# Optimization experiments

Measured on AMD Instinct MI355X. Metric: run time of the kernel, lower is better.

The kernel has to match this reference:

```python
import jax, jax.numpy as jnp
import numpy as np

S_DIM = 4096
N_NODES = 4096
N_EDGES = 32768


def _coarsen(ei_np, N):
    """Integer-only greedy coarsening, faithful to MNGRAPH.forward's while-loop.
    Returns (select order, flattened neighbor indices, segment ids, per-hub
    neighbor counts, forward-fill indices replicating the stale-M behavior for
    empty neighborhoods, and the remapped final edge_index)."""
    ei = ei_np.astype(np.int64).copy()
    I = np.bincount(ei[0], minlength=N)
    O = np.bincount(ei[1], minlength=N)
    order = np.argsort(-(I + O), kind='stable')  # torch.argsort(D, descending=True)
    visits = np.zeros(N, dtype=bool)
    select = []
    nbr_idx, nbr_seg, counts = [], [], []
    while order.size > 0:
        node = int(order[0])
        select.append(node)
        visits[node] = True
        # H = unique neighbors of node in the CURRENT (rewritten) edge_index
        H = np.unique(np.concatenate([ei[1][ei[0] == node], ei[0][ei[1] == node]]))
        visits[H] = True
        order = order[~visits[order]]
        # rewrite: endpoints in H that are not already-selected hubs -> node
        Hn = H[~np.isin(H, np.asarray(select, dtype=np.int64))]
        ei[np.isin(ei, Hn)] = node
        ei = ei[:, ei[0] != ei[1]]  # drop self-loops
        # append reversed edges that are not already present (pair-code isin
        # == the original O(E^2) all/any comparison, computed efficiently)
        code = ei[0] * N + ei[1]
        rcode = ei[1] * N + ei[0]
        new = ~np.isin(rcode, code)
        ei = np.concatenate([ei, ei[::-1][:, new]], axis=1)
        k = len(select) - 1
        nbr_idx.append(H)
        nbr_seg.append(np.full(H.shape[0], k, dtype=np.int64))
        counts.append(H.shape[0])
    select = np.asarray(select, dtype=np.int64)
    sort_sel = np.sort(select)
    ei_out = np.searchsorted(sort_sel, ei)  # compact node ids
    counts = np.asarray(counts, dtype=np.int64)
    # forward-fill: when H is empty the original appends the previous (stale) M
    fill = np.arange(select.shape[0])
    for i in range(select.shape[0]):
        if counts[i] == 0:
            fill[i] = fill[i - 1] if i > 0 else 0
    nbr = np.concatenate(nbr_idx) if nbr_idx else np.zeros(0, np.int64)
    seg = np.concatenate(nbr_seg) if nbr_seg else np.zeros(0, np.int64)
    return select, nbr, seg, counts, fill, ei_out


def setup_inputs() -> dict:
    key = jax.random.key(0)
    k1, k2, k3, k4 = jax.random.split(key, 4)
    x = jax.random.normal(k1, (N_NODES, S_DIM), dtype=jnp.float32)
    edge_index = jax.random.randint(k2, (2, N_EDGES), 0, N_NODES, dtype=jnp.int64)
    bound = float(np.sqrt(6.0 / (1.0 + S_DIM)))  # xavier_uniform on (1, S)
    W1 = jax.random.uniform(k3, (S_DIM,), jnp.float32, -bound, bound)
    W2 = jax.random.uniform(k4, (S_DIM,), jnp.float32, -bound, bound)
    B1 = jnp.zeros((S_DIM,), jnp.float32)
    B2 = jnp.zeros((S_DIM,), jnp.float32)
    return {"x": x, "edge_index": edge_index, "W1": W1, "W2": W2, "B1": B1, "B2": B2}


def reference(x, edge_index, W1, W2, B1, B2):
    N = x.shape[0]
    sel, nbr, seg, counts, fill, ei_out = _coarsen(np.asarray(edge_index), N)
    K = sel.shape[0]
    # Dn = x[n]*W1+B1 for every neighbor of every hub; per-hub mean via segment_sum
    Dn = x[jnp.asarray(nbr)] * W1 + B1                      # [T, S]
    sums = jax.ops.segment_sum(Dn, jnp.asarray(seg), num_segments=K)
    denom = jnp.maximum(jnp.asarray(counts), 1).astype(x.dtype)[:, None]
    mean_Dn = sums / denom                                  # [K, S]
    Dv = x[jnp.asarray(sel)] * W2 + B2                      # [K, S]
    END = jnp.concatenate([Dv, mean_Dn], axis=1)            # [K, 2S]
    END = END[jnp.asarray(fill)]                            # stale-M replication
    return END, jnp.asarray(ei_out)
```

## Files before the change

kernel.cpp:

```cpp
#include <hip/hip_runtime.h>
#include <hip/hip_bf16.h>

#define NT 1024
#define NNODES 4096
#define ECAP 65536

__global__ __launch_bounds__(256)
void zeroBM(int4* __restrict__ bm) {
    bm[(size_t)blockIdx.x * 256 + threadIdx.x] = make_int4(0, 0, 0, 0);
}

__device__ __forceinline__ int blockScanExcl(int v, int* s_w, int* total) {
    const int tid  = threadIdx.x;
    const int lane = tid & 63;
    const int wv   = tid >> 6;
    int x = v;
#pragma unroll
    for (int off = 1; off < 64; off <<= 1) {
        int t = __shfl_up(x, off, 64);
        if (lane >= off) x += t;
    }
    if (lane == 63) s_w[wv] = x;
    __syncthreads();
    if (tid < 16) {
        int y = s_w[tid];
#pragma unroll
        for (int off = 1; off < 16; off <<= 1) {
            int t = __shfl_up(y, off, 16);
            if (tid >= off) y += t;
        }
        s_w[tid] = y;
    }
    __syncthreads();
    int base = wv ? s_w[wv - 1] : 0;
    int tot  = s_w[15];
    __syncthreads();
    *total = tot;
    return base + x - v;
}

__global__ __launch_bounds__(NT, 1)
void phaseA1(const int* __restrict__ ei, int E0,
             int* __restrict__ U, int* __restrict__ V,
             unsigned int* __restrict__ BM,
             int* __restrict__ NBR, int* __restrict__ OTH,
             int* __restrict__ ORDV, int* __restrict__ ROFFG, int* __restrict__ RENDG,
             int* __restrict__ HAND)
{
    __shared__ unsigned short s_order[NNODES];
    __shared__ unsigned char  s_vis[NNODES];
    __shared__ unsigned char  s_rank[NNODES];
    __shared__ unsigned int   s_hb[NNODES / 32];
    __shared__ int s_roff[NNODES];
    __shared__ int s_rend[NNODES];
    __shared__ int s_tmp[NNODES];
    __shared__ int s_mat[64][65];
    __shared__ int s_w[16];
    __shared__ int s_bc[16];

    const int tid = threadIdx.x;

    for (int i = tid; i < NNODES; i += NT) { s_vis[i] = 0; s_tmp[i] = 0; }
    for (int i = tid; i < NNODES / 32; i += NT) s_hb[i] = 0;
    if (tid < 16) s_bc[tid] = 0;
    __syncthreads();

    for (int i = tid; i < E0; i += NT)
        if (ei[2 * i + 1] != 0) s_bc[9] = 1;
    __syncthreads();
    const int is64 = !s_bc[9];

    for (int e = tid; e < E0; e += NT) {
        int uu = ei[is64 ? 2 * e : e];
        int vv = ei[is64 ? 2 * (E0 + e) : (E0 + e)];
        U[e] = uu; V[e] = vv;
        atomicAdd(&s_tmp[uu], 1);
        atomicAdd(&s_tmp[vv], 1);
    }
    __syncthreads();
    for (int n = tid; n < NNODES; n += NT) atomicMax(&s_bc[7], s_tmp[n]);
    __syncthreads();
    const int maxd = s_bc[7];

    if (maxd < 64) {
        const int wv = tid >> 6, lane = tid & 63;
        const unsigned long long ltm = (1ull << lane) - 1ull;
        for (int g = wv; g < 64; g += 16) {
            int n = g * 64 + lane;
            int d = s_tmp[n];
            int rk = 0;
            for (int dd = 0; dd < 64; ++dd) {
                unsigned long long bal = __ballot(d == dd);
                if (lane == 0) s_mat[dd][g] = __popcll(bal);
                if (d == dd) rk = __popcll(bal & ltm);
            }
            s_rank[n] = (unsigned char)rk;
        }
        __syncthreads();
        if (tid < 64) {
            int run = 0;
            for (int g = 0; g < 64; ++g) { int t = s_mat[tid][g]; s_mat[tid][g] = run; run += t; }
            s_mat[tid][64] = run;
        }
        __syncthreads();
        if (tid < 64) {
            int x = s_mat[tid][64];
#pragma unroll
            for (int off = 1; off < 64; off <<= 1) {
                int t = __shfl_up(x, off, 64);
                if (tid >= off) x += t;
            }
            int T = __shfl(x, 63, 64);
            s_mat[tid][64] = T - x;
        }
        __syncthreads();
        for (int g = wv; g < 64; g += 16) {
            int n = g * 64 + lane;
            int d = s_tmp[n];
            int pos = s_mat[d][64] + s_mat[d][g] + (int)s_rank[n];
            s_order[pos] = (unsigned short)n;
        }
        __syncthreads();
    } else {
        for (int d = maxd; d >= 0; --d) {
            int n0 = tid * 4;
            int f0 = (s_tmp[n0] == d), f1 = (s_tmp[n0 + 1] == d);
            int f2 = (s_tmp[n0 + 2] == d), f3 = (s_tmp[n0 + 3] == d);
            int tot;
            int off = blockScanExcl(f0 + f1 + f2 + f3, s_w, &tot);
            int idx = s_bc[4] + off;
            if (f0) s_order[idx++] = (unsigned short)n0;
            if (f1) s_order[idx++] = (unsigned short)(n0 + 1);
            if (f2) s_order[idx++] = (unsigned short)(n0 + 2);
            if (f3) s_order[idx++] = (unsigned short)(n0 + 3);
            __syncthreads();
            if (tid == 0) s_bc[4] += tot;
            __syncthreads();
        }
    }

    if (tid == 0) {
        int nd = s_order[0];
        s_bc[0] = nd; s_vis[nd] = 1;
    }
    __syncthreads();
    {
        const int node = s_bc[0];
        for (int e = tid; e < E0; e += NT) {
            int uu = U[e], vv = V[e];
            if (uu == node) {
                int w = vv; unsigned m = 1u << (w & 31);
                unsigned old = atomicOr(&s_hb[w >> 5], m);
                if (!(old & m)) { int i = atomicAdd(&s_bc[2], 1); s_tmp[i] = w; s_vis[w] = 1; }
            }
            if (vv == node) {
                int w = uu; unsigned m = 1u << (w & 31);
                unsigned old = atomicOr(&s_hb[w >> 5], m);
                if (!(old & m)) { int i = atomicAdd(&s_bc[2], 1); s_tmp[i] = w; s_vis[w] = 1; }
            }
        }
        __syncthreads();
        for (int e = tid; e < E0; e += NT) {
            int uu = U[e];
            if (uu != node && ((s_hb[uu >> 5] >> (uu & 31)) & 1)) U[e] = node;
            int vv = V[e];
            if (vv != node && ((s_hb[vv >> 5] >> (vv & 31)) & 1)) V[e] = node;
        }
        __syncthreads();
    }

    for (int e = tid; e < E0; e += NT) {
        int uu = U[e], vv = V[e];
        if (uu != vv) {
            unsigned code = ((unsigned)uu << 12) | (unsigned)vv;
            atomicOr(&BM[code >> 5], 1u << (code & 31));
        }
    }
    __syncthreads();
    for (int t0 = 0; t0 < E0; t0 += NT * 32) {
        unsigned fm = 0u;
        const int base = t0 + tid * 32;
        for (int j = 0; j < 32; ++j) {
            int e = base + j;
            if (e < E0) {
                int uu = U[e], vv = V[e];
                if (uu != vv) {
                    unsigned rc = ((unsigned)vv << 12) | (unsigned)uu;
                    unsigned old = atomicOr(&BM[rc >> 5], 0u);
                    if (!((old >> (rc & 31)) & 1u)) fm |= (1u << j);
                }
            }
        }
        int tot;
        int off = blockScanExcl(__popc(fm), s_w, &tot);
        int r = s_bc[5] + off;
        unsigned m = fm;
        while (m) {
            int j = __ffs((int)m) - 1; m &= m - 1;
            int e = base + j;
            U[E0 + r] = V[e]; V[E0 + r] = U[e];
            ++r;
        }
        __syncthreads();
        if (tid == 0) s_bc[5] += tot;
        __syncthreads();
    }
    const int E1 = E0 + s_bc[5];

    for (int n = tid; n < NNODES; n += NT) s_roff[n] = 0;
    __syncthreads();
    for (int e = tid; e < E1; e += NT) {
        int uu = U[e], vv = V[e];
        if (uu != vv) atomicAdd(&s_roff[uu], 1);
    }
    __syncthreads();
    {
        int n0 = tid * 4;
        int c0 = s_roff[n0], c1 = s_roff[n0 + 1], c2 = s_roff[n0 + 2], c3 = s_roff[n0 + 3];
        int tot;
        int off = blockScanExcl(c0 + c1 + c2 + c3, s_w, &tot);
        int st = off;
        s_roff[n0] = st;     s_rend[n0] = st;     st += c0;
        s_roff[n0 + 1] = st; s_rend[n0 + 1] = st; st += c1;
        s_roff[n0 + 2] = st; s_rend[n0 + 2] = st; st += c2;
        s_roff[n0 + 3] = st; s_rend[n0 + 3] = st;
    }
    __syncthreads();
    for (int e = tid; e < E1; e += NT) {
        int uu = U[e], vv = V[e];
        if (uu != vv) {
            int p = atomicAdd(&s_rend[uu], 1);
            OTH[p] = vv;
        }
    }
    __syncthreads();
    {
        const int cnt0 = s_bc[2];
        for (int i = tid; i < cnt0; i += NT) NBR[i] = s_tmp[i];
    }
    for (int i = tid; i < NNODES; i += NT) {
        int nd = (int)s_order[i];
        ORDV[i]  = nd | (s_vis[nd] ? 0x8000 : 0);
        ROFFG[i] = s_roff[i];
        RENDG[i] = s_rend[i];
    }
    if (tid == 0) { HAND[0] = E1; HAND[1] = s_bc[2]; HAND[2] = s_bc[0]; }
}

__global__ __launch_bounds__(64, 1)
void phaseA2(const int* __restrict__ OTH, int* __restrict__ NBR,
             const int* __restrict__ ORDV, const int* __restrict__ ROFFG,
             const int* __restrict__ RENDG, const int* __restrict__ HAND,
             int* __restrict__ SEL, int* __restrict__ CNTS,
             int* __restrict__ NST, int* __restrict__ FIL, int* __restrict__ SC,
             int* __restrict__ LABG, int* __restrict__ RNKG)
{
    __shared__ unsigned short s_ord[NNODES];
    __shared__ unsigned int   s_visbits[NNODES / 32];
    __shared__ unsigned int   s_meta[NNODES];
    __shared__ unsigned short s_so[NNODES];
    __shared__ int s_cnt[NNODES];
    __shared__ int s_stamp[NNODES];
    __shared__ int s_roff[NNODES];
    __shared__ int s_rend[NNODES];

    const int ln = threadIdx.x;
    const unsigned long long ltm = (1ull << ln) - 1ull;
    const int cnt0 = HAND[1], hub0 = HAND[2];
    volatile int* vstamp = s_stamp;

    for (int i = ln; i < NNODES / 32; i += 64) s_visbits[i] = 0u;
    for (int i = ln; i < NNODES; i += 64) {
        int ov = ORDV[i];
        int nd = ov & 0x7FFF;
        s_ord[i] = (unsigned short)nd;
        s_meta[nd] = ((unsigned)i << 16) | (unsigned)nd;
        s_roff[i] = ROFFG[i];
        s_rend[i] = RENDG[i];
        s_stamp[i] = 0; s_cnt[i] = 0;
        if (ov & 0x8000) atomicOr(&s_visbits[i >> 5], 1u << (i & 31));
    }
    if (ln == 0) {
        s_meta[hub0] = (unsigned)hub0 | 0x8000u;
        s_so[0] = (unsigned short)hub0;
        s_cnt[0] = cnt0;
    }

    int nc = cnt0;
    int k = 1;

    unsigned lo = 0u, hi = 0u;
    auto reload = [&]() { lo = ~s_visbits[ln]; hi = ~s_visbits[ln + 64]; };
    auto extract = [&]() -> int {
        unsigned long long b = __ballot(lo != 0u);
        if (b) {
            int sl = __ffsll((long long)b) - 1;
            unsigned ww = __shfl(lo, sl, 64);
            if (ln == sl) lo &= lo - 1;
            return sl * 32 + (__ffs((int)ww) - 1);
        }
        b = __ballot(hi != 0u);
        if (b) {
            int sl = __ffsll((long long)b) - 1;
            unsigned ww = __shfl(hi, sl, 64);
            if (ln == sl) hi &= hi - 1;
            return 2048 + sl * 32 + (__ffs((int)ww) - 1);
        }
        return -1;
    };

    auto commitNew = [&](unsigned g, int w, bool nw, unsigned long long bal,
                         unsigned relv) {
        if (nw) {
            NBR[nc + __popcll(bal & ltm)] = w;
            int slot = (int)(g >> 16);
            atomicOr(&s_visbits[slot >> 5], 1u << (slot & 31));
            if (!(g & 0x8000u)) s_meta[w] = relv;
        }
        nc += __popcll(bal);
    };

    auto procFast = [&](int hub, int hslot, int o, unsigned g) {
        const unsigned relv = ((unsigned)hslot << 16) | (unsigned)hub | 0x8000u;
        int w = (o >= 0) ? (int)(g & 0x7FFFu) : hub;
        bool valid = (o >= 0) && (w != hub);
        if (valid) vstamp[w] = ln;
        int r = valid ? vstamp[w] : -1;
        bool nw = valid && (r == ln);
        unsigned long long bal = __ballot(nw);
        commitNew(g, w, nw, bal, relv);
    };

    auto procSlow = [&](int hub, int hslot, int rb, int re, int o0) {
        const unsigned relv = ((unsigned)hslot << 16) | (unsigned)hub | 0x8000u;
        const int key = k << 6;
        int o = o0;
        for (int s0 = rb; s0 < re; s0 += 64) {
            unsigned g = (o >= 0) ? s_meta[o] : 0u;
            int w = (o >= 0) ? (int)(g & 0x7FFFu) : hub;
            bool cnd = (w != hub);
            int old = key;
            if (cnd) old = atomicMax(&s_stamp[w], key);
            bool nw = cnd && (old < key);
            unsigned long long bal = __ballot(nw);
            commitNew(g, w, nw, bal, relv);
            int s1 = s0 + 64;
            o = (s1 + ln < re) ? OTH[s1 + ln] : -1;
        }
    };

    for (;;) {
        reload();
        int sl0 = extract();
        if (sl0 < 0) break;
        int sl1 = extract(), sl2 = -1, sl3 = -1;
        if (sl1 >= 0) { sl2 = extract(); if (sl2 >= 0) sl3 = extract(); }

        int c0 = (int)s_ord[sl0];
        int c1 = (sl1 >= 0) ? (int)s_ord[sl1] : -1;
        int c2 = (sl2 >= 0) ? (int)s_ord[sl2] : -1;
        int c3 = (sl3 >= 0) ? (int)s_ord[sl3] : -1;

        {
            int ms = (ln == 0) ? sl0 : (ln == 1) ? sl1 : (ln == 2) ? sl2 : sl3;
            if (ln < 4 && ms >= 0) atomicOr(&s_visbits[ms >> 5], 1u << (ms & 31));
        }

        int rb0 = s_roff[c0], re0 = s_rend[c0];
        int rb1 = 0, re1 = 0, rb2 = 0, re2 = 0, rb3 = 0, re3 = 0;
        if (c1 >= 0) { rb1 = s_roff[c1]; re1 = s_rend[c1]; }
        if (c2 >= 0) { rb2 = s_roff[c2]; re2 = s_rend[c2]; }
        if (c3 >= 0) { rb3 = s_roff[c3]; re3 = s_rend[c3]; }
        int v0 = (rb0 + ln < re0) ? OTH[rb0 + ln] : -1;
        int v1 = (c1 >= 0 && rb1 + ln < re1) ? OTH[rb1 + ln] : -1;
        int v2 = (c2 >= 0 && rb2 + ln < re2) ? OTH[rb2 + ln] : -1;
        int v3 = (c3 >= 0 && rb3 + ln < re3) ? OTH[rb3 + ln] : -1;

        if (ln == 0) {
            s_meta[c0] = ((unsigned)sl0 << 16) | (unsigned)c0 | 0x8000u;
            s_so[k] = (unsigned short)c0;
        }
        {
            unsigned g0 = (v0 >= 0) ? s_meta[v0] : 0u;
            int begin = nc;
            if (re0 - rb0 <= 64) procFast(c0, sl0, v0, g0);
            else                 procSlow(c0, sl0, rb0, re0, v0);
            if (ln == 0) s_cnt[k] = nc - begin;
            k++;
        }
        if (c1 >= 0) {
            unsigned m1 = s_meta[c1];
            unsigned g1 = (v1 >= 0) ? s_meta[v1] : 0u;
            if ((int)(m1 & 0x7FFFu) == c1) {
                if (ln == 0) {
                    s_meta[c1] = ((unsigned)sl1 << 16) | (unsigned)c1 | 0x8000u;
                    s_so[k] = (unsigned short)c1;
                }
                int begin = nc;
                if (re1 - rb1 <= 64) procFast(c1, sl1, v1, g1);
                else                 procSlow(c1, sl1, rb1, re1, v1);
                if (ln == 0) s_cnt[k] = nc - begin;
                k++;
            }
        }
        if (c2 >= 0) {
            unsigned m2 = s_meta[c2];
            unsigned g2 = (v2 >= 0) ? s_meta[v2] : 0u;
            if ((int)(m2 & 0x7FFFu) == c2) {
                if (ln == 0) {
                    s_meta[c2] = ((unsigned)sl2 << 16) | (unsigned)c2 | 0x8000u;
                    s_so[k] = (unsigned short)c2;
                }
                int begin = nc;
                if (re2 - rb2 <= 64) procFast(c2, sl2, v2, g2);
                else                 procSlow(c2, sl2, rb2, re2, v2);
                if (ln == 0) s_cnt[k] = nc - begin;
                k++;
            }
        }
        if (c3 >= 0) {
            unsigned m3 = s_meta[c3];
            unsigned g3 = (v3 >= 0) ? s_meta[v3] : 0u;
            if ((int)(m3 & 0x7FFFu) == c3) {
                if (ln == 0) {
                    s_meta[c3] = ((unsigned)sl3 << 16) | (unsigned)c3 | 0x8000u;
                    s_so[k] = (unsigned short)c3;
                }
                int begin = nc;
                if (re3 - rb3 <= 64) procFast(c3, sl3, v3, g3);
                else                 procSlow(c3, sl3, rb3, re3, v3);
                if (ln == 0) s_cnt[k] = nc - begin;
                k++;
            }
        }
    }
    const int K = k;

    {
        int base = 0;
        for (int c = 0; c < NNODES / 64; ++c) {
            int n = c * 64 + ln;
            unsigned mv = s_meta[n];
            int f = ((mv & 0x8000u) != 0u) && ((int)(mv & 0x7FFFu) == n);
            unsigned long long b = __ballot(f);
            s_stamp[n] = base + __popcll(b & ltm);
            base += __popcll(b);
        }
    }
    {
        int nb = 0;
        for (int c = 0; c * 64 < K; ++c) {
            int i = c * 64 + ln;
            int cv = (i < K) ? s_cnt[i] : 0;
            int x = cv;
#pragma unroll
            for (int off = 1; off < 64; off <<= 1) {
                int t = __shfl_up(x, off, 64);
                if (ln >= off) x += t;
            }
            if (i < K) { NST[i] = nb + x - cv; CNTS[i] = cv; SEL[i] = (int)s_so[i]; }
            nb += __shfl(x, 63, 64);
        }
    }
    {
        int carry = 0;
        for (int c = 0; c * 64 < K; ++c) {
            int i = c * 64 + ln;
            int f = (i < K) && (s_cnt[i] > 0);
            unsigned long long b = __ballot(f);
            unsigned long long m = b & ((ln == 63) ? ~0ull : ((1ull << (ln + 1)) - 1ull));
            int fil = m ? (c * 64 + 63 - __clzll(m)) : carry;
            if (i < K) FIL[i] = fil;
            carry = b ? (c * 64 + 63 - __clzll(b)) : carry;
        }
    }
    if (ln == 0) SC[0] = K;
    for (int i = ln; i < NNODES; i += 64) {
        LABG[i] = (int)(s_meta[i] & 0x7FFFu);
        RNKG[i] = s_stamp[i];
    }
}

__global__ __launch_bounds__(NT, 1)
void phaseA3(const int* __restrict__ U, const int* __restrict__ V,
             const int* __restrict__ LABG, const int* __restrict__ RNKG,
             const int* __restrict__ HAND, int* __restrict__ SC,
             int* __restrict__ TMP, float* __restrict__ out)
{
    __shared__ unsigned short l_lab[NNODES];
    __shared__ int l_rnk[NNODES];
    __shared__ int s_w[16];
    __shared__ int s_base[1];

    const int tid = threadIdx.x;
    for (int i = tid; i < NNODES; i += NT) {
        l_lab[i] = (unsigned short)LABG[i];
        l_rnk[i] = RNKG[i];
    }
    if (tid == 0) s_base[0] = 0;
    __syncthreads();

    const int E1 = HAND[0];
    const int K  = SC[0];
    const size_t obase = (size_t)K * 8192;

    for (int t0 = 0; t0 < E1; t0 += NT * 64) {
        unsigned long long fm = 0ull;
        const int base = t0 + tid * 64;
        if (base + 64 <= E1) {
            const int4* U4 = (const int4*)(U + base);
            const int4* V4 = (const int4*)(V + base);
#pragma unroll
            for (int q = 0; q < 16; ++q) {
                int4 a = U4[q], b = V4[q];
                int j = q * 4;
                if ((int)l_lab[a.x] != (int)l_lab[b.x]) fm |= 1ull << j;
                if ((int)l_lab[a.y] != (int)l_lab[b.y]) fm |= 1ull << (j + 1);
                if ((int)l_lab[a.z] != (int)l_lab[b.z]) fm |= 1ull << (j + 2);
                if ((int)l_lab[a.w] != (int)l_lab[b.w]) fm |= 1ull << (j + 3);
            }
        } else {
            for (int j = 0; j < 64; ++j) {
                int e = base + j;
                if (e < E1) {
                    if ((int)l_lab[U[e]] != (int)l_lab[V[e]]) fm |= 1ull << j;
                }
            }
        }
        int tot;
        int off = blockScanExcl(__popcll(fm), s_w, &tot);
        int r = s_base[0] + off;
        unsigned long long m = fm;
        while (m) {
            int j = __ffsll((long long)m) - 1; m &= m - 1;
            int e = base + j;
            out[obase + (size_t)r] = (float)l_rnk[(int)l_lab[U[e]]];
            TMP[r] = l_rnk[(int)l_lab[V[e]]];
            ++r;
        }
        __syncthreads();
        if (tid == 0) s_base[0] += tot;
        __syncthreads();
    }
    const int Ef = s_base[0];
    if (tid == 0) SC[1] = Ef;
    for (int r = tid; r < Ef; r += NT)
        out[obase + (size_t)Ef + (size_t)r] = (float)TMP[r];
}

__global__ __launch_bounds__(256, 4)
void phaseB(const float* __restrict__ x,
            const float* __restrict__ W1, const float* __restrict__ W2,
            const float* __restrict__ B1, const float* __restrict__ B2,
            const int* __restrict__ NBR, const int* __restrict__ SEL,
            const int* __restrict__ CNTS, const int* __restrict__ NST,
            const int* __restrict__ FIL, const int* __restrict__ SC,
            float* __restrict__ out)
{
    const int K = SC[0];
    const int k = blockIdx.x;
    if (k >= K) return;
    const int kk   = FIL[k];
    const int node = SEL[kk];
    const int cnt  = CNTS[kk];
    const int st   = NST[kk];
    const int tid  = threadIdx.x;
    const float4* x4 = (const float4*)x;

    float4 acc[4];
#pragma unroll
    for (int j = 0; j < 4; j++) acc[j] = make_float4(0.f, 0.f, 0.f, 0.f);

    for (int r = 0; r < cnt; ++r) {
        const float4* row = x4 + (size_t)NBR[st + r] * 1024;
#pragma unroll
        for (int j = 0; j < 4; j++) {
            float4 t = row[tid + j * 256];
            acc[j].x += t.x; acc[j].y += t.y; acc[j].z += t.z; acc[j].w += t.w;
        }
    }

    const float fc  = (float)cnt;
    const float inv = 1.0f / (float)(cnt > 1 ? cnt : 1);
    const float4* xr = x4 + (size_t)node * 1024;
    float4* o4 = (float4*)(out + (size_t)k * 8192);

#pragma unroll
    for (int j = 0; j < 4; j++) {
        int c = tid + j * 256;
        float4 w1 = ((const float4*)W1)[c], b1 = ((const float4*)B1)[c];
        float4 w2 = ((const float4*)W2)[c], b2 = ((const float4*)B2)[c];
        float4 xv = xr[c];
        float4 pd, pm;
        pd.x = xv.x * w2.x + b2.x;
        pd.y = xv.y * w2.y + b2.y;
        pd.z = xv.z * w2.z + b2.z;
        pd.w = xv.w * w2.w + b2.w;
        pm.x = (acc[j].x * w1.x + fc * b1.x) * inv;
        pm.y = (acc[j].y * w1.y + fc * b1.y) * inv;
        pm.z = (acc[j].z * w1.z + fc * b1.z) * inv;
        pm.w = (acc[j].w * w1.w + fc * b1.w) * inv;
        o4[c] = pd;
        o4[1024 + c] = pm;
    }
}

extern "C" void kernel_launch(void* const* d_in, const int* in_sizes, int n_in,
                              void* d_out, int out_size, void* d_ws, size_t ws_size,
                              hipStream_t stream)
{
    const float* x  = (const float*)d_in[0];
    const int*   ei = (const int*)d_in[1];
    const float* W1 = (const float*)d_in[2];
    const float* W2 = (const float*)d_in[3];
    const float* B1 = (const float*)d_in[4];
    const float* B2 = (const float*)d_in[5];
    const int E0 = in_sizes[1] / 2;

    char* w = (char*)d_ws;
    int* U = (int*)w;
    int* V = U + ECAP;
    unsigned int* BM = (unsigned int*)(V + ECAP);
    int* OTH = (int*)BM;
    int* NBR = OTH + 2 * ECAP;
    int* TMP = NBR + 2 * ECAP;
    char* meta = (char*)BM + (2u << 20);
    int* SEL   = (int*)meta;
    int* CNTS  = SEL  + NNODES;
    int* NST   = CNTS + NNODES;
    int* FIL   = NST  + NNODES;
    int* SC    = FIL  + NNODES;
    int* ORDV  = SC   + 16;
    int* ROFFG = ORDV + NNODES;
    int* RENDG = ROFFG + NNODES;
    int* LABG  = RENDG + NNODES;
    int* RNKG  = LABG + NNODES;
    int* HAND  = RNKG + NNODES;
    float* out = (float*)d_out;

    hipLaunchKernelGGL(zeroBM, dim3(512), dim3(256), 0, stream, (int4*)BM);

    hipLaunchKernelGGL(phaseA1, dim3(1), dim3(NT), 0, stream,
                       ei, E0, U, V, BM, NBR, OTH, ORDV, ROFFG, RENDG, HAND);
    hipLaunchKernelGGL(phaseA2, dim3(1), dim3(64), 0, stream,
                       OTH, NBR, ORDV, ROFFG, RENDG, HAND,
                       SEL, CNTS, NST, FIL, SC, LABG, RNKG);
    hipLaunchKernelGGL(phaseA3, dim3(1), dim3(NT), 0, stream,
                       U, V, LABG, RNKG, HAND, SC, TMP, out);
    hipLaunchKernelGGL(phaseB, dim3(NNODES), dim3(256), 0, stream,
                       x, W1, W2, B1, B2, NBR, SEL, CNTS, NST, FIL, SC, out);
}
```

Baseline: 1.005 ms.

## Fuse three single-block coarsening kernels into one phaseA kernel with shared state

```diff
diff --git a/kernel.cpp b/kernel.cpp
--- a/kernel.cpp
+++ b/kernel.cpp
@@ -1,7 +1,8 @@
 #include <hip/hip_runtime.h>
 #include <hip/hip_bf16.h>
 
-#define NT 1024
+#define NT 512
+#define NW (NT / 64)
 #define NNODES 4096
 #define ECAP 65536
 
@@ -23,7 +24,7 @@
     if (lane == 63) s_w[wv] = x;
     __syncthreads();
     if (tid < 16) {
-        int y = s_w[tid];
+        int y = (tid < NW) ? s_w[tid] : 0;
 #pragma unroll
         for (int off = 1; off < 16; off <<= 1) {
             int t = __shfl_up(y, off, 16);
@@ -40,28 +41,33 @@
 }
 
 __global__ __launch_bounds__(NT, 1)
-void phaseA1(const int* __restrict__ ei, int E0,
-             int* __restrict__ U, int* __restrict__ V,
-             unsigned int* __restrict__ BM,
-             int* __restrict__ NBR, int* __restrict__ OTH,
-             int* __restrict__ ORDV, int* __restrict__ ROFFG, int* __restrict__ RENDG,
-             int* __restrict__ HAND)
+void phaseA(const int* __restrict__ ei, int E0,
+            int* __restrict__ U, int* __restrict__ V,
+            unsigned int* __restrict__ BM,
+            int* __restrict__ NBR, int* __restrict__ OTH,
+            int* __restrict__ SEL, int* __restrict__ CNTS,
+            int* __restrict__ NST, int* __restrict__ FIL, int* __restrict__ SC,
+            int* __restrict__ TMP, float* __restrict__ out)
 {
-    __shared__ unsigned short s_order[NNODES];
-    __shared__ unsigned char  s_vis[NNODES];
+    __shared__ unsigned short s_ord[NNODES];
+    __shared__ unsigned short s_pos[NNODES];
+    __shared__ unsigned short s_so[NNODES];
     __shared__ unsigned char  s_rank[NNODES];
+    __shared__ unsigned int   s_visbits[NNODES / 32];
     __shared__ unsigned int   s_hb[NNODES / 32];
+    __shared__ unsigned int   s_meta[NNODES];
+    __shared__ int s_mat[64][65];
     __shared__ int s_roff[NNODES];
     __shared__ int s_rend[NNODES];
-    __shared__ int s_tmp[NNODES];
-    __shared__ int s_mat[64][65];
+    __shared__ int s_stamp[NNODES];
+    __shared__ int s_degcnt[NNODES];
     __shared__ int s_w[16];
     __shared__ int s_bc[16];
 
     const int tid = threadIdx.x;
 
-    for (int i = tid; i < NNODES; i += NT) { s_vis[i] = 0; s_tmp[i] = 0; }
-    for (int i = tid; i < NNODES / 32; i += NT) s_hb[i] = 0;
+    for (int i = tid; i < NNODES; i += NT) s_degcnt[i] = 0;
+    for (int i = tid; i < NNODES / 32; i += NT) { s_hb[i] = 0u; s_visbits[i] = 0u; }
     if (tid < 16) s_bc[tid] = 0;
     __syncthreads();
 
@@ -74,25 +80,25 @@
         int uu = ei[is64 ? 2 * e : e];
         int vv = ei[is64 ? 2 * (E0 + e) : (E0 + e)];
         U[e] = uu; V[e] = vv;
-        atomicAdd(&s_tmp[uu], 1);
-        atomicAdd(&s_tmp[vv], 1);
-    }
-    __syncthreads();
-    for (int n = tid; n < NNODES; n += NT) atomicMax(&s_bc[7], s_tmp[n]);
+        atomicAdd(&s_degcnt[uu], 1);
+        atomicAdd(&s_degcnt[vv], 1);
+    }
+    __syncthreads();
+    for (int n = tid; n < NNODES; n += NT) atomicMax(&s_bc[7], s_degcnt[n]);
     __syncthreads();
     const int maxd = s_bc[7];
 
     if (maxd < 64) {
         const int wv = tid >> 6, lane = tid & 63;
-        const unsigned long long ltm = (1ull << lane) - 1ull;
-        for (int g = wv; g < 64; g += 16) {
+        const unsigned long long wltm = (1ull << lane) - 1ull;
+        for (int g = wv; g < 64; g += NW) {
             int n = g * 64 + lane;
-            int d = s_tmp[n];
+            int d = s_degcnt[n];
             int rk = 0;
             for (int dd = 0; dd < 64; ++dd) {
                 unsigned long long bal = __ballot(d == dd);
                 if (lane == 0) s_mat[dd][g] = __popcll(bal);
-                if (d == dd) rk = __popcll(bal & ltm);
+                if (d == dd) rk = __popcll(bal & wltm);
             }
             s_rank[n] = (unsigned char)rk;
         }
@@ -114,34 +120,37 @@
             s_mat[tid][64] = T - x;
         }
         __syncthreads();
-        for (int g = wv; g < 64; g += 16) {
+        for (int g = wv; g < 64; g += NW) {
             int n = g * 64 + lane;
-            int d = s_tmp[n];
+            int d = s_degcnt[n];
             int pos = s_mat[d][64] + s_mat[d][g] + (int)s_rank[n];
-            s_order[pos] = (unsigned short)n;
+            s_ord[pos] = (unsigned short)n;
         }
         __syncthreads();
     } else {
         for (int d = maxd; d >= 0; --d) {
-            int n0 = tid * 4;
-            int f0 = (s_tmp[n0] == d), f1 = (s_tmp[n0 + 1] == d);
-            int f2 = (s_tmp[n0 + 2] == d), f3 = (s_tmp[n0 + 3] == d);
+            const int n0 = tid * 8;
+            int f[8], cnt = 0;
+#pragma unroll
+            for (int q = 0; q < 8; ++q) { f[q] = (s_degcnt[n0 + q] == d); cnt += f[q]; }
             int tot;
-            int off = blockScanExcl(f0 + f1 + f2 + f3, s_w, &tot);
+            int off = blockScanExcl(cnt, s_w, &tot);
             int idx = s_bc[4] + off;
-            if (f0) s_order[idx++] = (unsigned short)n0;
-            if (f1) s_order[idx++] = (unsigned short)(n0 + 1);
-            if (f2) s_order[idx++] = (unsigned short)(n0 + 2);
-            if (f3) s_order[idx++] = (unsigned short)(n0 + 3);
+#pragma unroll
+            for (int q = 0; q < 8; ++q)
+                if (f[q]) s_ord[idx++] = (unsigned short)(n0 + q);
             __syncthreads();
             if (tid == 0) s_bc[4] += tot;
             __syncthreads();
         }
     }
 
+    for (int i = tid; i < NNODES; i += NT) s_pos[s_ord[i]] = (unsigned short)i;
+    __syncthreads();
+
     if (tid == 0) {
-        int nd = s_order[0];
-        s_bc[0] = nd; s_vis[nd] = 1;
+        s_bc[0] = (int)s_ord[0];
+        atomicOr(&s_visbits[0], 1u);
     }
     __syncthreads();
     {
@@ -151,12 +160,22 @@
             if (uu == node) {
                 int w = vv; unsigned m = 1u << (w & 31);
                 unsigned old = atomicOr(&s_hb[w >> 5], m);
-                if (!(old & m)) { int i = atomicAdd(&s_bc[2], 1); s_tmp[i] = w; s_vis[w] = 1; }
+                if (!(old & m)) {
+                    int i = atomicAdd(&s_bc[2], 1);
+                    s_degcnt[i] = w;
+                    int sl = (int)s_pos[w];
+                    atomicOr(&s_visbits[sl >> 5], 1u << (sl & 31));
+                }
             }
             if (vv == node) {
                 int w = uu; unsigned m = 1u << (w & 31);
                 unsigned old = atomicOr(&s_hb[w >> 5], m);
-                if (!(old & m)) { int i = atomicAdd(&s_bc[2], 1); s_tmp[i] = w; s_vis[w] = 1; }
+                if (!(old & m)) {
+                    int i = atomicAdd(&s_bc[2], 1);
+                    s_degcnt[i] = w;
+                    int sl = (int)s_pos[w];
+                    atomicOr(&s_visbits[sl >> 5], 1u << (sl & 31));
+                }
             }
         }
         __syncthreads();
@@ -215,15 +234,17 @@
     }
     __syncthreads();
     {
-        int n0 = tid * 4;
-        int c0 = s_roff[n0], c1 = s_roff[n0 + 1], c2 = s_roff[n0 + 2], c3 = s_roff[n0 + 3];
+        const int n0 = tid * 8;
+        int c[8], s = 0;
+#pragma unroll
+        for (int q = 0; q < 8; ++q) { c[q] = s_roff[n0 + q]; s += c[q]; }
         int tot;
-        int off = blockScanExcl(c0 + c1 + c2 + c3, s_w, &tot);
+        int off = blockScanExcl(s, s_w, &tot);
         int st = off;
-        s_roff[n0] = st;     s_rend[n0] = st;     st += c0;
-        s_roff[n0 + 1] = st; s_rend[n0 + 1] = st; st += c1;
-        s_roff[n0 + 2] = st; s_rend[n0 + 2] = st; st += c2;
-        s_roff[n0 + 3] = st; s_rend[n0 + 3] = st;
+#pragma unroll
+        for (int q = 0; q < 8; ++q) {
+            s_roff[n0 + q] = st; s_rend[n0 + q] = st; st += c[q];
+        }
     }
     __syncthreads();
     for (int e = tid; e < E1; e += NT) {
@@ -234,274 +255,222 @@
         }
     }
     __syncthreads();
-    {
-        const int cnt0 = s_bc[2];
-        for (int i = tid; i < cnt0; i += NT) NBR[i] = s_tmp[i];
-    }
+    const int cnt0 = s_bc[2];
+    for (int i = tid; i < cnt0; i += NT) NBR[i] = s_degcnt[i];
+    __syncthreads();
+
     for (int i = tid; i < NNODES; i += NT) {
-        int nd = (int)s_order[i];
-        ORDV[i]  = nd | (s_vis[nd] ? 0x8000 : 0);
-        ROFFG[i] = s_roff[i];
-        RENDG[i] = s_rend[i];
-    }
-    if (tid == 0) { HAND[0] = E1; HAND[1] = s_bc[2]; HAND[2] = s_bc[0]; }
-}
-
-__global__ __launch_bounds__(64, 1)
-void phaseA2(const int* __restrict__ OTH, int* __restrict__ NBR,
-             const int* __restrict__ ORDV, const int* __restrict__ ROFFG,
-             const int* __restrict__ RENDG, const int* __restrict__ HAND,
-             int* __restrict__ SEL, int* __restrict__ CNTS,
-             int* __restrict__ NST, int* __restrict__ FIL, int* __restrict__ SC,
-             int* __restrict__ LABG, int* __restrict__ RNKG)
-{
-    __shared__ unsigned short s_ord[NNODES];
-    __shared__ unsigned int   s_visbits[NNODES / 32];
-    __shared__ unsigned int   s_meta[NNODES];
-    __shared__ unsigned short s_so[NNODES];
-    __shared__ int s_cnt[NNODES];
-    __shared__ int s_stamp[NNODES];
-    __shared__ int s_roff[NNODES];
-    __shared__ int s_rend[NNODES];
-
-    const int ln = threadIdx.x;
-    const unsigned long long ltm = (1ull << ln) - 1ull;
-    const int cnt0 = HAND[1], hub0 = HAND[2];
-    volatile int* vstamp = s_stamp;
-
-    for (int i = ln; i < NNODES / 32; i += 64) s_visbits[i] = 0u;
-    for (int i = ln; i < NNODES; i += 64) {
-        int ov = ORDV[i];
-        int nd = ov & 0x7FFF;
-        s_ord[i] = (unsigned short)nd;
+        int nd = (int)s_ord[i];
         s_meta[nd] = ((unsigned)i << 16) | (unsigned)nd;
-        s_roff[i] = ROFFG[i];
-        s_rend[i] = RENDG[i];
-        s_stamp[i] = 0; s_cnt[i] = 0;
-        if (ov & 0x8000) atomicOr(&s_visbits[i >> 5], 1u << (i & 31));
-    }
-    if (ln == 0) {
+        s_stamp[i] = 0;
+        s_degcnt[i] = 0;
+    }
+    __syncthreads();
+    if (tid == 0) {
+        int hub0 = s_bc[0];
         s_meta[hub0] = (unsigned)hub0 | 0x8000u;
         s_so[0] = (unsigned short)hub0;
-        s_cnt[0] = cnt0;
-    }
-
-    int nc = cnt0;
-    int k = 1;
-
-    unsigned lo = 0u, hi = 0u;
-    auto reload = [&]() { lo = ~s_visbits[ln]; hi = ~s_visbits[ln + 64]; };
-    auto extract = [&]() -> int {
-        unsigned long long b = __ballot(lo != 0u);
-        if (b) {
-            int sl = __ffsll((long long)b) - 1;
-            unsigned ww = __shfl(lo, sl, 64);
-            if (ln == sl) lo &= lo - 1;
-            return sl * 32 + (__ffs((int)ww) - 1);
-        }
-        b = __ballot(hi != 0u);
-        if (b) {
-            int sl = __ffsll((long long)b) - 1;
-            unsigned ww = __shfl(hi, sl, 64);
-            if (ln == sl) hi &= hi - 1;
-            return 2048 + sl * 32 + (__ffs((int)ww) - 1);
-        }
-        return -1;
-    };
-
-    auto commitNew = [&](unsigned g, int w, bool nw, unsigned long long bal,
-                         unsigned relv) {
-        if (nw) {
-            NBR[nc + __popcll(bal & ltm)] = w;
-            int slot = (int)(g >> 16);
-            atomicOr(&s_visbits[slot >> 5], 1u << (slot & 31));
-            if (!(g & 0x8000u)) s_meta[w] = relv;
-        }
-        nc += __popcll(bal);
-    };
-
-    auto procFast = [&](int hub, int hslot, int o, unsigned g) {
-        const unsigned relv = ((unsigned)hslot << 16) | (unsigned)hub | 0x8000u;
-        int w = (o >= 0) ? (int)(g & 0x7FFFu) : hub;
-        bool valid = (o >= 0) && (w != hub);
-        if (valid) vstamp[w] = ln;
-        int r = valid ? vstamp[w] : -1;
-        bool nw = valid && (r == ln);
-        unsigned long long bal = __ballot(nw);
-        commitNew(g, w, nw, bal, relv);
-    };
-
-    auto procSlow = [&](int hub, int hslot, int rb, int re, int o0) {
-        const unsigned relv = ((unsigned)hslot << 16) | (unsigned)hub | 0x8000u;
-        const int key = k << 6;
-        int o = o0;
-        for (int s0 = rb; s0 < re; s0 += 64) {
-            unsigned g = (o >= 0) ? s_meta[o] : 0u;
+        s_degcnt[0] = cnt0;
+    }
+    __syncthreads();
+
+    if (tid < 64) {
+        const int ln = tid;
+        const unsigned long long ltm = (1ull << ln) - 1ull;
+        volatile int* vstamp = s_stamp;
+
+        int nc = cnt0;
+        int k = 1;
+
+        unsigned lo = 0u, hi = 0u;
+        auto extract = [&]() -> int {
+            unsigned long long b = __ballot(lo != 0u);
+            if (b) {
+                int sl = __ffsll((long long)b) - 1;
+                unsigned ww = __shfl(lo, sl, 64);
+                if (ln == sl) lo &= lo - 1;
+                return sl * 32 + (__ffs((int)ww) - 1);
+            }
+            b = __ballot(hi != 0u);
+            if (b) {
+                int sl = __ffsll((long long)b) - 1;
+                unsigned ww = __shfl(hi, sl, 64);
+                if (ln == sl) hi &= hi - 1;
+                return 2048 + sl * 32 + (__ffs((int)ww) - 1);
+            }
+            return -1;
+        };
+
+        auto commitNew = [&](unsigned g, int w, bool nw, unsigned long long bal,
+                             unsigned relv) {
+            if (nw) {
+                NBR[nc + __popcll(bal & ltm)] = w;
+                int slot = (int)(g >> 16);
+                atomicOr(&s_visbits[slot >> 5], 1u << (slot & 31));
+                if (!(g & 0x8000u)) s_meta[w] = relv;
+            }
+            nc += __popcll(bal);
+        };
+
+        auto procFast = [&](int hub, int hslot, int o, unsigned g) {
+            const unsigned relv = ((unsigned)hslot << 16) | (unsigned)hub | 0x8000u;
             int w = (o >= 0) ? (int)(g & 0x7FFFu) : hub;
-            bool cnd = (w != hub);
-            int old = key;
-            if (cnd) old = atomicMax(&s_stamp[w], key);
-            bool nw = cnd && (old < key);
+            bool valid = (o >= 0) && (w != hub);
+            if (valid) vstamp[w] = ln;
+            int r = valid ? vstamp[w] : -1;
+            bool nw = valid && (r == ln);
             unsigned long long bal = __ballot(nw);
             commitNew(g, w, nw, bal, relv);
-            int s1 = s0 + 64;
-            o = (s1 + ln < re) ? OTH[s1 + ln] : -1;
-        }
-    };
-
-    for (;;) {
-        reload();
-        int sl0 = extract();
-        if (sl0 < 0) break;
-        int sl1 = extract(), sl2 = -1, sl3 = -1;
-        if (sl1 >= 0) { sl2 = extract(); if (sl2 >= 0) sl3 = extract(); }
-
-        int c0 = (int)s_ord[sl0];
-        int c1 = (sl1 >= 0) ? (int)s_ord[sl1] : -1;
-        int c2 = (sl2 >= 0) ? (int)s_ord[sl2] : -1;
-        int c3 = (sl3 >= 0) ? (int)s_ord[sl3] : -1;
+        };
+
+        auto procSlow = [&](int hub, int hslot, int rb, int re, int o0) {
+            const unsigned relv = ((unsigned)hslot << 16) | (unsigned)hub | 0x8000u;
+            const int key = k << 6;
+            int o = o0;
+            for (int s0 = rb; s0 < re; s0 += 64) {
+                unsigned g = (o >= 0) ? s_meta[o] : 0u;
+                int w = (o >= 0) ? (int)(g & 0x7FFFu) : hub;
+                bool cnd = (w != hub);
+                int old = key;
+                if (cnd) old = atomicMax(&s_stamp[w], key);
+                bool nw = cnd && (old < key);
+                unsigned long long bal = __ballot(nw);
+                commitNew(g, w, nw, bal, relv);
+                int s1 = s0 + 64;
+                o = (s1 + ln < re) ? OTH[s1 + ln] : -1;
+            }
+        };
+
+        for (;;) {
+            lo = ~s_visbits[ln]; hi = ~s_visbits[ln + 64];
+            int sl0 = extract();
+            if (sl0 < 0) break;
+            int sl1 = extract(), sl2 = -1, sl3 = -1;
+            if (sl1 >= 0) { sl2 = extract(); if (sl2 >= 0) sl3 = extract(); }
+
+            int c0 = (int)s_ord[sl0];
+            int c1 = (sl1 >= 0) ? (int)s_ord[sl1] : -1;
+            int c2 = (sl2 >= 0) ? (int)s_ord[sl2] : -1;
+            int c3 = (sl3 >= 0) ? (int)s_ord[sl3] : -1;
+
+            {
+                int ms = (ln == 0) ? sl0 : (ln == 1) ? sl1 : (ln == 2) ? sl2 : sl3;
+                if (ln < 4 && ms >= 0) atomicOr(&s_visbits[ms >> 5], 1u << (ms & 31));
+            }
+
+            int rb0 = s_roff[c0], re0 = s_rend[c0];
+            int rb1 = 0, re1 = 0, rb2 = 0, re2 = 0, rb3 = 0, re3 = 0;
+            if (c1 >= 0) { rb1 = s_roff[c1]; re1 = s_rend[c1]; }
+            if (c2 >= 0) { rb2 = s_roff[c2]; re2 = s_rend[c2]; }
+            if (c3 >= 0) { rb3 = s_roff[c3]; re3 = s_rend[c3]; }
+            int v0 = (rb0 + ln < re0) ? OTH[rb0 + ln] : -1;
+            int v1 = (c1 >= 0 && rb1 + ln < re1) ? OTH[rb1 + ln] : -1;
+            int v2 = (c2 >= 0 && rb2 + ln < re2) ? OTH[rb2 + ln] : -1;
+            int v3 = (c3 >= 0 && rb3 + ln < re3) ? OTH[rb3 + ln] : -1;
+
+            if (ln == 0) {
+                s_meta[c0] = ((unsigned)sl0 << 16) | (unsigned)c0 | 0x8000u;
+                s_so[k] = (unsigned short)c0;
+            }
+            {
+                unsigned g0 = (v0 >= 0) ? s_meta[v0] : 0u;
+                int begin = nc;
+                if (re0 - rb0 <= 64) procFast(c0, sl0, v0, g0);
+                else                 procSlow(c0, sl0, rb0, re0, v0);
+                if (ln == 0) s_degcnt[k] = nc - begin;
+                k++;
+            }
+            if (c1 >= 0) {
+                unsigned m1 = s_meta[c1];
+                unsigned g1 = (v1 >= 0) ? s_meta[v1] : 0u;
+                if ((int)(m1 & 0x7FFFu) == c1) {
+                    if (ln == 0) {
+                        s_meta[c1] = ((unsigned)sl1 << 16) | (unsigned)c1 | 0x8000u;
+                        s_so[k] = (unsigned short)c1;
+                    }
+                    int begin = nc;
+                    if (re1 - rb1 <= 64) procFast(c1, sl1, v1, g1);
+                    else                 procSlow(c1, sl1, rb1, re1, v1);
+                    if (ln == 0) s_degcnt[k] = nc - begin;
+                    k++;
+                }
+            }
+            if (c2 >= 0) {
+                unsigned m2 = s_meta[c2];
+                unsigned g2 = (v2 >= 0) ? s_meta[v2] : 0u;
+                if ((int)(m2 & 0x7FFFu) == c2) {
+                    if (ln == 0) {
+                        s_meta[c2] = ((unsigned)sl2 << 16) | (unsigned)c2 | 0x8000u;
+                        s_so[k] = (unsigned short)c2;
+                    }
+                    int begin = nc;
+                    if (re2 - rb2 <= 64) procFast(c2, sl2, v2, g2);
+                    else                 procSlow(c2, sl2, rb2, re2, v2);
+                    if (ln == 0) s_degcnt[k] = nc - begin;
+                    k++;
+                }
+            }
+            if (c3 >= 0) {
+                unsigned m3 = s_meta[c3];
+                unsigned g3 = (v3 >= 0) ? s_meta[v3] : 0u;
+                if ((int)(m3 & 0x7FFFu) == c3) {
+                    if (ln == 0) {
+                        s_meta[c3] = ((unsigned)sl3 << 16) | (unsigned)c3 | 0x8000u;
+                        s_so[k] = (unsigned short)c3;
+                    }
+                    int begin = nc;
+                    if (re3 - rb3 <= 64) procFast(c3, sl3, v3, g3);
+                    else                 procSlow(c3, sl3, rb3, re3, v3);
+                    if (ln == 0) s_degcnt[k] = nc - begin;
+                    k++;
+                }
+            }
+        }
+        const int K = k;
 
         {
-            int ms = (ln == 0) ? sl0 : (ln == 1) ? sl1 : (ln == 2) ? sl2 : sl3;
-            if (ln < 4 && ms >= 0) atomicOr(&s_visbits[ms >> 5], 1u << (ms & 31));
-        }
-
-        int rb0 = s_roff[c0], re0 = s_rend[c0];
-        int rb1 = 0, re1 = 0, rb2 = 0, re2 = 0, rb3 = 0, re3 = 0;
-        if (c1 >= 0) { rb1 = s_roff[c1]; re1 = s_rend[c1]; }
-        if (c2 >= 0) { rb2 = s_roff[c2]; re2 = s_rend[c2]; }
-        if (c3 >= 0) { rb3 = s_roff[c3]; re3 = s_rend[c3]; }
-        int v0 = (rb0 + ln < re0) ? OTH[rb0 + ln] : -1;
-        int v1 = (c1 >= 0 && rb1 + ln < re1) ? OTH[rb1 + ln] : -1;
-        int v2 = (c2 >= 0 && rb2 + ln < re2) ? OTH[rb2 + ln] : -1;
-        int v3 = (c3 >= 0 && rb3 + ln < re3) ? OTH[rb3 + ln] : -1;
-
-        if (ln == 0) {
-            s_meta[c0] = ((unsigned)sl0 << 16) | (unsigned)c0 | 0x8000u;
-            s_so[k] = (unsigned short)c0;
+            int base = 0;
+            for (int c = 0; c < NNODES / 64; ++c) {
+                int n = c * 64 + ln;
+                unsigned mv = s_meta[n];
+                int f = ((mv & 0x8000u) != 0u) && ((int)(mv & 0x7FFFu) == n);
+                unsigned long long b = __ballot(f);
+                s_stamp[n] = base + __popcll(b & ltm);
+                base += __popcll(b);
+            }
         }
         {
-            unsigned g0 = (v0 >= 0) ? s_meta[v0] : 0u;
-            int begin = nc;
-            if (re0 - rb0 <= 64) procFast(c0, sl0, v0, g0);
-            else                 procSlow(c0, sl0, rb0, re0, v0);
-            if (ln == 0) s_cnt[k] = nc - begin;
-            k++;
-        }
-        if (c1 >= 0) {
-            unsigned m1 = s_meta[c1];
-            unsigned g1 = (v1 >= 0) ? s_meta[v1] : 0u;
-            if ((int)(m1 & 0x7FFFu) == c1) {
-                if (ln == 0) {
-                    s_meta[c1] = ((unsigned)sl1 << 16) | (unsigned)c1 | 0x8000u;
-                    s_so[k] = (unsigned short)c1;
-                }
-                int begin = nc;
-                if (re1 - rb1 <= 64) procFast(c1, sl1, v1, g1);
-                else                 procSlow(c1, sl1, rb1, re1, v1);
-                if (ln == 0) s_cnt[k] = nc - begin;
-                k++;
-            }
-        }
-        if (c2 >= 0) {
-            unsigned m2 = s_meta[c2];
-            unsigned g2 = (v2 >= 0) ? s_meta[v2] : 0u;
-            if ((int)(m2 & 0x7FFFu) == c2) {
-                if (ln == 0) {
-                    s_meta[c2] = ((unsigned)sl2 << 16) | (unsigned)c2 | 0x8000u;
-                    s_so[k] = (unsigned short)c2;
-                }
-                int begin = nc;
-                if (re2 - rb2 <= 64) procFast(c2, sl2, v2, g2);
-                else                 procSlow(c2, sl2, rb2, re2, v2);
-                if (ln == 0) s_cnt[k] = nc - begin;
-                k++;
-            }
-        }
-        if (c3 >= 0) {
-            unsigned m3 = s_meta[c3];
-            unsigned g3 = (v3 >= 0) ? s_meta[v3] : 0u;
-            if ((int)(m3 & 0x7FFFu) == c3) {
-                if (ln == 0) {
-                    s_meta[c3] = ((unsigned)sl3 << 16) | (unsigned)c3 | 0x8000u;
-                    s_so[k] = (unsigned short)c3;
-                }
-                int begin = nc;
-                if (re3 - rb3 <= 64) procFast(c3, sl3, v3, g3);
-                else                 procSlow(c3, sl3, rb3, re3, v3);
-                if (ln == 0) s_cnt[k] = nc - begin;
-                k++;
-            }
-        }
-    }
-    const int K = k;
-
-    {
-        int base = 0;
-        for (int c = 0; c < NNODES / 64; ++c) {
-            int n = c * 64 + ln;
-            unsigned mv = s_meta[n];
-            int f = ((mv & 0x8000u) != 0u) && ((int)(mv & 0x7FFFu) == n);
-            unsigned long long b = __ballot(f);
-            s_stamp[n] = base + __popcll(b & ltm);
-            base += __popcll(b);
-        }
-    }
-    {
-        int nb = 0;
-        for (int c = 0; c * 64 < K; ++c) {
-            int i = c * 64 + ln;
-            int cv = (i < K) ? s_cnt[i] : 0;
-            int x = cv;
-#pragma unroll
-            for (int off = 1; off < 64; off <<= 1) {
-                int t = __shfl_up(x, off, 64);
-                if (ln >= off) x += t;
-            }
-            if (i < K) { NST[i] = nb + x - cv; CNTS[i] = cv; SEL[i] = (int)s_so[i]; }
-            nb += __shfl(x, 63, 64);
-        }
-    }
-    {
-        int carry = 0;
-        for (int c = 0; c * 64 < K; ++c) {
-            int i = c * 64 + ln;
-            int f = (i < K) && (s_cnt[i] > 0);
-            unsigned long long b = __ballot(f);
-            unsigned long long m = b & ((ln == 63) ? ~0ull : ((1ull << (ln + 1)) - 1ull));
-            int fil = m ? (c * 64 + 63 - __clzll(m)) : carry;
-            if (i < K) FIL[i] = fil;
-            carry = b ? (c * 64 + 63 - __clzll(b)) : carry;
-        }
-    }
-    if (ln == 0) SC[0] = K;
-    for (int i = ln; i < NNODES; i += 64) {
-        LABG[i] = (int)(s_meta[i] & 0x7FFFu);
-        RNKG[i] = s_stamp[i];
-    }
-}
-
-__global__ __launch_bounds__(NT, 1)
-void phaseA3(const int* __restrict__ U, const int* __restrict__ V,
-             const int* __restrict__ LABG, const int* __restrict__ RNKG,
-             const int* __restrict__ HAND, int* __restrict__ SC,
-             int* __restrict__ TMP, float* __restrict__ out)
-{
-    __shared__ unsigned short l_lab[NNODES];
-    __shared__ int l_rnk[NNODES];
-    __shared__ int s_w[16];
-    __shared__ int s_base[1];
-
-    const int tid = threadIdx.x;
-    for (int i = tid; i < NNODES; i += NT) {
-        l_lab[i] = (unsigned short)LABG[i];
-        l_rnk[i] = RNKG[i];
-    }
-    if (tid == 0) s_base[0] = 0;
-    __syncthreads();
-
-    const int E1 = HAND[0];
-    const int K  = SC[0];
+            int nb = 0;
+            for (int c = 0; c * 64 < K; ++c) {
+                int i = c * 64 + ln;
+                int cv = (i < K) ? s_degcnt[i] : 0;
+                int x = cv;
+#pragma unroll
+                for (int off = 1; off < 64; off <<= 1) {
+                    int t = __shfl_up(x, off, 64);
+                    if (ln >= off) x += t;
+                }
+                if (i < K) { NST[i] = nb + x - cv; CNTS[i] = cv; SEL[i] = (int)s_so[i]; }
+                nb += __shfl(x, 63, 64);
+            }
+        }
+        {
+            int carry = 0;
+            for (int c = 0; c * 64 < K; ++c) {
+                int i = c * 64 + ln;
+                int f = (i < K) && (s_degcnt[i] > 0);
+                unsigned long long b = __ballot(f);
+                unsigned long long m = b & ((ln == 63) ? ~0ull : ((1ull << (ln + 1)) - 1ull));
+                int fil = m ? (c * 64 + 63 - __clzll(m)) : carry;
+                if (i < K) FIL[i] = fil;
+                carry = b ? (c * 64 + 63 - __clzll(b)) : carry;
+            }
+        }
+        if (ln == 0) { SC[0] = K; s_bc[3] = K; }
+    }
+    __syncthreads();
+
+    const int K = s_bc[3];
     const size_t obase = (size_t)K * 8192;
 
     for (int t0 = 0; t0 < E1; t0 += NT * 64) {
@@ -514,35 +483,35 @@
             for (int q = 0; q < 16; ++q) {
                 int4 a = U4[q], b = V4[q];
                 int j = q * 4;
-                if ((int)l_lab[a.x] != (int)l_lab[b.x]) fm |= 1ull << j;
-                if ((int)l_lab[a.y] != (int)l_lab[b.y]) fm |= 1ull << (j + 1);
-                if ((int)l_lab[a.z] != (int)l_lab[b.z]) fm |= 1ull << (j + 2);
-                if ((int)l_lab[a.w] != (int)l_lab[b.w]) fm |= 1ull << (j + 3);
+                if ((s_meta[a.x] ^ s_meta[b.x]) & 0x7FFFu) fm |= 1ull << j;
+                if ((s_meta[a.y] ^ s_meta[b.y]) & 0x7FFFu) fm |= 1ull << (j + 1);
+                if ((s_meta[a.z] ^ s_meta[b.z]) & 0x7FFFu) fm |= 1ull << (j + 2);
+                if ((s_meta[a.w] ^ s_meta[b.w]) & 0x7FFFu) fm |= 1ull << (j + 3);
             }
         } else {
             for (int j = 0; j < 64; ++j) {
                 int e = base + j;
                 if (e < E1) {
-                    if ((int)l_lab[U[e]] != (int)l_lab[V[e]]) fm |= 1ull << j;
+                    if ((s_meta[U[e]] ^ s_meta[V[e]]) & 0x7FFFu) fm |= 1ull << j;
                 }
             }
         }
         int tot;
         int off = blockScanExcl(__popcll(fm), s_w, &tot);
-        int r = s_base[0] + off;
+        int r = s_bc[10] + off;
         unsigned long long m = fm;
         while (m) {
             int j = __ffsll((long long)m) - 1; m &= m - 1;
             int e = base + j;
-            out[obase + (size_t)r] = (float)l_rnk[(int)l_lab[U[e]]];
-            TMP[r] = l_rnk[(int)l_lab[V[e]]];
+            out[obase + (size_t)r] = (float)s_stamp[(int)(s_meta[U[e]] & 0x7FFFu)];
+            TMP[r] = s_stamp[(int)(s_meta[V[e]] & 0x7FFFu)];
             ++r;
         }
         __syncthreads();
-        if (tid == 0) s_base[0] += tot;
-        __syncthreads();
-    }
-    const int Ef = s_base[0];
+        if (tid == 0) s_bc[10] += tot;
+        __syncthreads();
+    }
+    const int Ef = s_bc[10];
     if (tid == 0) SC[1] = Ef;
     for (int r = tid; r < Ef; r += NT)
         out[obase + (size_t)Ef + (size_t)r] = (float)TMP[r];
@@ -630,23 +599,14 @@
     int* NST   = CNTS + NNODES;
     int* FIL   = NST  + NNODES;
     int* SC    = FIL  + NNODES;
-    int* ORDV  = SC   + 16;
-    int* ROFFG = ORDV + NNODES;
-    int* RENDG = ROFFG + NNODES;
-    int* LABG  = RENDG + NNODES;
-    int* RNKG  = LABG + NNODES;
-    int* HAND  = RNKG + NNODES;
     float* out = (float*)d_out;
 
     hipLaunchKernelGGL(zeroBM, dim3(512), dim3(256), 0, stream, (int4*)BM);
 
-    hipLaunchKernelGGL(phaseA1, dim3(1), dim3(NT), 0, stream,
-                       ei, E0, U, V, BM, NBR, OTH, ORDV, ROFFG, RENDG, HAND);
-    hipLaunchKernelGGL(phaseA2, dim3(1), dim3(64), 0, stream,
-                       OTH, NBR, ORDV, ROFFG, RENDG, HAND,
-                       SEL, CNTS, NST, FIL, SC, LABG, RNKG);
-    hipLaunchKernelGGL(phaseA3, dim3(1), dim3(NT), 0, stream,
-                       U, V, LABG, RNKG, HAND, SC, TMP, out);
+    hipLaunchKernelGGL(phaseA, dim3(1), dim3(NT), 0, stream,
+                       ei, E0, U, V, BM, NBR, OTH,
+                       SEL, CNTS, NST, FIL, SC, TMP, out);
+
     hipLaunchKernelGGL(phaseB, dim3(NNODES), dim3(256), 0, stream,
                        x, W1, W2, B1, B2, NBR, SEL, CNTS, NST, FIL, SC, out);
 }
```

Result: slower. 1.039 ms (+3.4%).
